# Performance work log

Hardware: AMD Instinct MI355X
Metric: run time of the kernel (lower is better)

Reference implementation:

```python
import jax, jax.numpy as jnp
import numpy as np

N = 8192
F_IN = 128
F_OUT = 128
NEG_SLOPE = 0.2


def setup_inputs() -> dict:
    key = jax.random.key(0)
    k_h, k_adj, k_W, k_a = jax.random.split(key, 4)
    h = jax.random.normal(k_h, (N, F_IN), dtype=jnp.float32)
    # binary adjacency mask as float (the module multiplies scores by adj)
    adj = (jax.random.uniform(k_adj, (N, N)) < 0.05).astype(jnp.float32)
    # nn.Linear(in, out, bias=False): weight shape [out, in]
    W = jax.random.normal(k_W, (F_OUT, F_IN), dtype=jnp.float32) / np.sqrt(F_IN)
    # nn.Linear(2*out, 1, bias=False): weight shape [1, 2*out]
    a = jax.random.normal(k_a, (1, 2 * F_OUT), dtype=jnp.float32) / np.sqrt(2 * F_OUT)
    return {"h": h, "adj": adj, "W": W, "a": a}


def reference(h, adj, W, a):
    # Wh: [N, F_out]
    Wh = h @ W.T
    f = Wh.shape[-1]
    # a([Wh_i ; Wh_j]) factored: e[i, j] = leaky_relu(Wh[i]@a1 + Wh[j]@a2)
    a1 = a[0, :f]  # [F_out]
    a2 = a[0, f:]  # [F_out]
    s_i = Wh @ a1  # [N]
    s_j = Wh @ a2  # [N]
    e = jax.nn.leaky_relu(s_i[:, None] + s_j[None, :], NEG_SLOPE)  # [N, N]
    # faithful to original: softmax over dim=1 of e * adj (multiplicative mask)
    attention = jax.nn.softmax(e * adj, axis=1)  # [N, N]
    return attention @ Wh  # [N, F_out]
```

## Files before the change

### kernel.cpp

```cpp
#include <hip/hip_runtime.h>

#define N_NODES 8192
#define FDIM 128
#define NEG_SLOPE 0.2f
#define SEG 512

__device__ __forceinline__ unsigned int f2bf(float f) {
  unsigned int u = __float_as_uint(f);
  return (u + 0x7FFFu + ((u >> 16) & 1u)) >> 16;
}

__global__ __launch_bounds__(256) void wh_fused_kernel(
    const float* __restrict__ h, const float* __restrict__ W,
    const float* __restrict__ a,
    unsigned int* __restrict__ Whb,
    float* __restrict__ s1, float* __restrict__ s2,
    float* __restrict__ S) {
  __shared__ float Wt[FDIM * 132];
  __shared__ float rows[32 * 132];
  const int t = threadIdx.x;
  const int base = blockIdx.x * 32;
  for (int it = 0; it < 64; ++it) {
    int idx = t + 256 * it;
    int o = idx >> 7, k = idx & 127;
    Wt[k * 132 + o] = W[idx];
  }
  for (int it = 0; it < 16; ++it) {
    int idx = t + 256 * it;
    int r = idx >> 7, col = idx & 127;
    rows[r * 132 + col] = h[(size_t)base * FDIM + idx];
  }
  __syncthreads();
  const int c4 = (t & 31) * 4;
  const int g = t >> 5;
  float acc[4][4];
#pragma unroll
  for (int rr = 0; rr < 4; ++rr)
#pragma unroll
    for (int cc = 0; cc < 4; ++cc) acc[rr][cc] = 0.f;
  for (int k = 0; k < FDIM; ++k) {
    float4 wv = *(const float4*)&Wt[k * 132 + c4];
    float rv[4];
#pragma unroll
    for (int rr = 0; rr < 4; ++rr) rv[rr] = rows[(4 * g + rr) * 132 + k];
#pragma unroll
    for (int rr = 0; rr < 4; ++rr) {
      acc[rr][0] += rv[rr] * wv.x;
      acc[rr][1] += rv[rr] * wv.y;
      acc[rr][2] += rv[rr] * wv.z;
      acc[rr][3] += rv[rr] * wv.w;
    }
  }
#pragma unroll
  for (int rr = 0; rr < 4; ++rr) {
    int r = base + 4 * g + rr;
    unsigned int p0 = f2bf(acc[rr][0]) | (f2bf(acc[rr][1]) << 16);
    unsigned int p1 = f2bf(acc[rr][2]) | (f2bf(acc[rr][3]) << 16);
    *(uint2*)&Whb[(size_t)r * 64 + (c4 >> 1)] = make_uint2(p0, p1);
  }
  {
    float4 a1v = *(const float4*)&a[c4];
    float4 a2v = *(const float4*)&a[FDIM + c4];
#pragma unroll
    for (int rr = 0; rr < 4; ++rr) {
      float d1 = acc[rr][0] * a1v.x + acc[rr][1] * a1v.y +
                 acc[rr][2] * a1v.z + acc[rr][3] * a1v.w;
      float d2 = acc[rr][0] * a2v.x + acc[rr][1] * a2v.y +
                 acc[rr][2] * a2v.z + acc[rr][3] * a2v.w;
#pragma unroll
      for (int off = 16; off; off >>= 1) {
        d1 += __shfl_down(d1, off);
        d2 += __shfl_down(d2, off);
      }
      if ((t & 31) == 0) {
        s1[base + 4 * g + rr] = d1;
        s2[base + 4 * g + rr] = d2;
      }
    }
  }
  __syncthreads();
  float4 cs = make_float4(acc[0][0] + acc[1][0] + acc[2][0] + acc[3][0],
                          acc[0][1] + acc[1][1] + acc[2][1] + acc[3][1],
                          acc[0][2] + acc[1][2] + acc[2][2] + acc[3][2],
                          acc[0][3] + acc[1][3] + acc[2][3] + acc[3][3]);
  *(float4*)&rows[g * FDIM + c4] = cs;
  __syncthreads();
  if (t < FDIM) {
    float s = 0.f;
#pragma unroll
    for (int gg = 0; gg < 8; ++gg) s += rows[gg * FDIM + t];
    atomicAdd(&S[t], s);
  }
}

__device__ __forceinline__ float4 ntload4(const float4* p) {
  typedef float f4v __attribute__((ext_vector_type(4)));
  f4v v = __builtin_nontemporal_load((const f4v*)p);
  return make_float4(v[0], v[1], v[2], v[3]);
}

__global__ __launch_bounds__(256, 4) void gat_row_kernel(
    const float* __restrict__ adj, const unsigned int* __restrict__ Whb,
    const float* __restrict__ s1, const float* __restrict__ s2,
    const float* __restrict__ S, float* __restrict__ out) {
  const int i = blockIdx.x;
  const int t = threadIdx.x;
  const int lane = t & 63;
  const int wave = t >> 6;
  __shared__ float2 pairs[4 * SEG];
  __shared__ int counts[4];
  __shared__ float red[4];
  __shared__ float red2[4];
  __shared__ float fpart[4][FDIM];

  const float s1i = s1[i];
  const float4* __restrict__ arow = (const float4*)(adj + (size_t)i * N_NODES);
  float2* __restrict__ mypairs = pairs + wave * SEG;
  const unsigned long long lmask = (1ull << lane) - 1ull;

  float4 av[8];
#pragma unroll
  for (int it = 0; it < 8; ++it) av[it] = ntload4(&arow[it * 256 + t]);
  asm volatile("" ::
      "v"(av[0].x), "v"(av[0].y), "v"(av[0].z), "v"(av[0].w),
      "v"(av[1].x), "v"(av[1].y), "v"(av[1].z), "v"(av[1].w),
      "v"(av[2].x), "v"(av[2].y), "v"(av[2].z), "v"(av[2].w),
      "v"(av[3].x), "v"(av[3].y), "v"(av[3].z), "v"(av[3].w),
      "v"(av[4].x), "v"(av[4].y), "v"(av[4].z), "v"(av[4].w),
      "v"(av[5].x), "v"(av[5].y), "v"(av[5].z), "v"(av[5].w),
      "v"(av[6].x), "v"(av[6].y), "v"(av[6].z), "v"(av[6].w),
      "v"(av[7].x), "v"(av[7].y), "v"(av[7].z), "v"(av[7].w));
  __builtin_amdgcn_sched_barrier(0);
  int cbase = 0;
#pragma unroll
  for (int it = 0; it < 8; ++it) {
    const int j4 = it * 256 + t;
    float v[4] = {av[it].x, av[it].y, av[it].z, av[it].w};
#pragma unroll
    for (int c = 0; c < 4; ++c) {
      bool pred = (v[c] != 0.f);
      unsigned long long b = __ballot(pred);
      if (pred) {
        int pos = cbase + (int)__popcll(b & lmask);
        if (pos < SEG) ((int*)&mypairs[pos])[1] = j4 * 4 + c;
      }
      cbase += (int)__popcll(b);
    }
  }
  const int mycnt = cbase < SEG ? cbase : SEG;
  if (lane == 0) counts[wave] = mycnt;

  float lmax = -1e30f;
  for (int k = lane; k < mycnt; k += 64) {
    int j = ((const int*)&mypairs[k])[1];
    float e = s1i + s2[j];
    e = e > 0.f ? e : NEG_SLOPE * e;
    mypairs[k].x = e;
    lmax = fmaxf(lmax, e);
  }
  for (int off = 32; off; off >>= 1) lmax = fmaxf(lmax, __shfl_down(lmax, off));
  if (lane == 0) red[wave] = lmax;
  __syncthreads();
  const int cnt = counts[0] + counts[1] + counts[2] + counts[3];
  float m = fmaxf(fmaxf(red[0], red[1]), fmaxf(red[2], red[3]));
  if (cnt < N_NODES) m = fmaxf(m, 0.f);
  const float em = __expf(-m);

  float lsum = 0.f;
  for (int k = lane; k < mycnt; k += 64) {
    float p = __expf(mypairs[k].x - m);
    mypairs[k].x = p;
    lsum += p;
  }
  for (int off = 32; off; off >>= 1) lsum += __shfl_down(lsum, off);
  if (lane == 0) red2[wave] = lsum;

  const int half = lane >> 5, lq = lane & 31;
  const uint2* __restrict__ Whb2 = (const uint2*)Whb;
  float ax = 0.f, ay = 0.f, az = 0.f, aw = 0.f;
  const int nit = (mycnt + 1) >> 1;
  int it = 0;
  for (; it + 3 < nit; it += 4) {
#pragma unroll
    for (int c = 0; c < 4; ++c) {
      int p = 2 * (it + c) + half;
      bool ok = p < mycnt;
      float2 pr = mypairs[ok ? p : 0];
      int j = ((const int*)&pr)[1];
      uint2 d = Whb2[((size_t)j << 5) + lq];
      float w = ok ? pr.x - em : 0.f;
      ax += w * __uint_as_float(d.x << 16);
      ay += w * __uint_as_float(d.x & 0xffff0000u);
      az += w * __uint_as_float(d.y << 16);
      aw += w * __uint_as_float(d.y & 0xffff0000u);
    }
  }
  for (; it < nit; ++it) {
    int p = 2 * it + half;
    bool ok = p < mycnt;
    float2 pr = mypairs[ok ? p : 0];
    int j = ((const int*)&pr)[1];
    uint2 d = Whb2[((size_t)j << 5) + lq];
    float w = ok ? pr.x - em : 0.f;
    ax += w * __uint_as_float(d.x << 16);
    ay += w * __uint_as_float(d.x & 0xffff0000u);
    az += w * __uint_as_float(d.y << 16);
    aw += w * __uint_as_float(d.y & 0xffff0000u);
  }
  ax += __shfl_down(ax, 32);
  ay += __shfl_down(ay, 32);
  az += __shfl_down(az, 32);
  aw += __shfl_down(aw, 32);
  if (lane < 32)
    *(float4*)&fpart[wave][4 * lq] = make_float4(ax, ay, az, aw);
  __syncthreads();
  if (t < FDIM) {
    float l = red2[0] + red2[1] + red2[2] + red2[3]
              + (float)(N_NODES - cnt) * em;
    float o = (fpart[0][t] + fpart[1][t] + fpart[2][t] + fpart[3][t]
               + em * S[t]) / l;
    out[(size_t)i * FDIM + t] = o;
  }
}

extern "C" void kernel_launch(void* const* d_in, const int* in_sizes, int n_in,
                              void* d_out, int out_size, void* d_ws, size_t ws_size,
                              hipStream_t stream) {
  const float* h   = (const float*)d_in[0];
  const float* adj = (const float*)d_in[1];
  const float* W   = (const float*)d_in[2];
  const float* a   = (const float*)d_in[3];
  float* out = (float*)d_out;
  unsigned int* Whb = (unsigned int*)d_ws;
  float* s1 = (float*)(Whb + (size_t)N_NODES * 64);
  float* s2 = s1 + N_NODES;
  float* S  = s2 + N_NODES;

  hipMemsetAsync(S, 0, FDIM * sizeof(float), stream);
  hipLaunchKernelGGL(wh_fused_kernel, dim3(N_NODES / 32), dim3(256), 0, stream,
                     h, W, a, Whb, s1, s2, S);
  hipLaunchKernelGGL(gat_row_kernel, dim3(N_NODES), dim3(256), 0, stream,
                     adj, Whb, s1, s2, S, out);
}
```

Before: 404.1 us.

## Fuse score computation into compaction and exp into aggregation; pre-transpose W

The row kernel now loads the whole s2 vector coalesced alongside the adjacency row and computes the leaky-relu scores and running max during the ballot compaction. This removes the separate gather pass over s2 and the separate exp/sum pass over the pair buffer, and the exp and sum now run inside the aggregation loop. The exp is evaluated once per half-wave lane, so lsum is scaled by 1/32. W is also transposed once in a small extra kernel so the projection kernel can use float4 loads. The cost is an extra 32 KB read of s2 per row and one more kernel launch.

```diff
diff --git a/kernel.cpp b/kernel.cpp
--- a/kernel.cpp
+++ b/kernel.cpp
@@ -10,8 +10,14 @@
   return (u + 0x7FFFu + ((u >> 16) & 1u)) >> 16;
 }
 
+__global__ __launch_bounds__(256) void transpose_w_kernel(
+    const float* __restrict__ W, float* __restrict__ WtG) {
+  int idx = blockIdx.x * 256 + threadIdx.x;
+  WtG[idx] = W[(idx & 127) * FDIM + (idx >> 7)];
+}
+
 __global__ __launch_bounds__(256) void wh_fused_kernel(
-    const float* __restrict__ h, const float* __restrict__ W,
+    const float* __restrict__ h, const float* __restrict__ WtG,
     const float* __restrict__ a,
     unsigned int* __restrict__ Whb,
     float* __restrict__ s1, float* __restrict__ s2,
@@ -20,15 +26,16 @@
   __shared__ float rows[32 * 132];
   const int t = threadIdx.x;
   const int base = blockIdx.x * 32;
-  for (int it = 0; it < 64; ++it) {
-    int idx = t + 256 * it;
-    int o = idx >> 7, k = idx & 127;
-    Wt[k * 132 + o] = W[idx];
-  }
   for (int it = 0; it < 16; ++it) {
     int idx = t + 256 * it;
-    int r = idx >> 7, col = idx & 127;
-    rows[r * 132 + col] = h[(size_t)base * FDIM + idx];
+    int k = idx >> 5, c = (idx & 31) * 4;
+    *(float4*)&Wt[k * 132 + c] = *(const float4*)&WtG[k * FDIM + c];
+  }
+  for (int it = 0; it < 4; ++it) {
+    int idx = t + 256 * it;
+    int r = idx >> 5, c = (idx & 31) * 4;
+    *(float4*)&rows[r * 132 + c] =
+        *(const float4*)&h[(size_t)(base + r) * FDIM + c];
   }
   __syncthreads();
   const int c4 = (t & 31) * 4;
@@ -97,6 +104,11 @@
   typedef float f4v __attribute__((ext_vector_type(4)));
   f4v v = __builtin_nontemporal_load((const f4v*)p);
   return make_float4(v[0], v[1], v[2], v[3]);
+}
+
+__device__ __forceinline__ int mbcnt64(unsigned long long b) {
+  return (int)__builtin_amdgcn_mbcnt_hi(
+      (unsigned)(b >> 32), __builtin_amdgcn_mbcnt_lo((unsigned)b, 0u));
 }
 
 __global__ __launch_bounds__(256, 4) void gat_row_kernel(
@@ -115,49 +127,42 @@
 
   const float s1i = s1[i];
   const float4* __restrict__ arow = (const float4*)(adj + (size_t)i * N_NODES);
+  const float4* __restrict__ srow = (const float4*)s2;
   float2* __restrict__ mypairs = pairs + wave * SEG;
-  const unsigned long long lmask = (1ull << lane) - 1ull;
-
-  float4 av[8];
+
+  float4 av[8], sv[8];
 #pragma unroll
   for (int it = 0; it < 8; ++it) av[it] = ntload4(&arow[it * 256 + t]);
-  asm volatile("" ::
-      "v"(av[0].x), "v"(av[0].y), "v"(av[0].z), "v"(av[0].w),
-      "v"(av[1].x), "v"(av[1].y), "v"(av[1].z), "v"(av[1].w),
-      "v"(av[2].x), "v"(av[2].y), "v"(av[2].z), "v"(av[2].w),
-      "v"(av[3].x), "v"(av[3].y), "v"(av[3].z), "v"(av[3].w),
-      "v"(av[4].x), "v"(av[4].y), "v"(av[4].z), "v"(av[4].w),
-      "v"(av[5].x), "v"(av[5].y), "v"(av[5].z), "v"(av[5].w),
-      "v"(av[6].x), "v"(av[6].y), "v"(av[6].z), "v"(av[6].w),
-      "v"(av[7].x), "v"(av[7].y), "v"(av[7].z), "v"(av[7].w));
-  __builtin_amdgcn_sched_barrier(0);
+#pragma unroll
+  for (int it = 0; it < 8; ++it) sv[it] = srow[it * 256 + t];
   int cbase = 0;
+  float lmax = -1e30f;
 #pragma unroll
   for (int it = 0; it < 8; ++it) {
     const int j4 = it * 256 + t;
-    float v[4] = {av[it].x, av[it].y, av[it].z, av[it].w};
+    float vv[4] = {av[it].x, av[it].y, av[it].z, av[it].w};
+    float ss[4] = {sv[it].x, sv[it].y, sv[it].z, sv[it].w};
 #pragma unroll
     for (int c = 0; c < 4; ++c) {
-      bool pred = (v[c] != 0.f);
+      bool pred = (vv[c] != 0.f);
+      float e = s1i + ss[c];
+      e = e > 0.f ? e : NEG_SLOPE * e;
       unsigned long long b = __ballot(pred);
       if (pred) {
-        int pos = cbase + (int)__popcll(b & lmask);
-        if (pos < SEG) ((int*)&mypairs[pos])[1] = j4 * 4 + c;
+        int pos = cbase + mbcnt64(b);
+        if (pos < SEG) {
+          float2 pr;
+          pr.x = e;
+          ((int*)&pr)[1] = j4 * 4 + c;
+          mypairs[pos] = pr;
+        }
       }
+      lmax = fmaxf(lmax, pred ? e : -1e30f);
       cbase += (int)__popcll(b);
     }
   }
   const int mycnt = cbase < SEG ? cbase : SEG;
   if (lane == 0) counts[wave] = mycnt;
-
-  float lmax = -1e30f;
-  for (int k = lane; k < mycnt; k += 64) {
-    int j = ((const int*)&mypairs[k])[1];
-    float e = s1i + s2[j];
-    e = e > 0.f ? e : NEG_SLOPE * e;
-    mypairs[k].x = e;
-    lmax = fmaxf(lmax, e);
-  }
   for (int off = 32; off; off >>= 1) lmax = fmaxf(lmax, __shfl_down(lmax, off));
   if (lane == 0) red[wave] = lmax;
   __syncthreads();
@@ -166,18 +171,9 @@
   if (cnt < N_NODES) m = fmaxf(m, 0.f);
   const float em = __expf(-m);
 
-  float lsum = 0.f;
-  for (int k = lane; k < mycnt; k += 64) {
-    float p = __expf(mypairs[k].x - m);
-    mypairs[k].x = p;
-    lsum += p;
-  }
-  for (int off = 32; off; off >>= 1) lsum += __shfl_down(lsum, off);
-  if (lane == 0) red2[wave] = lsum;
-
   const int half = lane >> 5, lq = lane & 31;
   const uint2* __restrict__ Whb2 = (const uint2*)Whb;
-  float ax = 0.f, ay = 0.f, az = 0.f, aw = 0.f;
+  float ax = 0.f, ay = 0.f, az = 0.f, aw = 0.f, lsum = 0.f;
   const int nit = (mycnt + 1) >> 1;
   int it = 0;
   for (; it + 3 < nit; it += 4) {
@@ -188,7 +184,9 @@
       float2 pr = mypairs[ok ? p : 0];
       int j = ((const int*)&pr)[1];
       uint2 d = Whb2[((size_t)j << 5) + lq];
-      float w = ok ? pr.x - em : 0.f;
+      float pv = __expf(pr.x - m);
+      float w = ok ? pv - em : 0.f;
+      lsum += ok ? pv : 0.f;
       ax += w * __uint_as_float(d.x << 16);
       ay += w * __uint_as_float(d.x & 0xffff0000u);
       az += w * __uint_as_float(d.y << 16);
@@ -201,12 +199,16 @@
     float2 pr = mypairs[ok ? p : 0];
     int j = ((const int*)&pr)[1];
     uint2 d = Whb2[((size_t)j << 5) + lq];
-    float w = ok ? pr.x - em : 0.f;
+    float pv = __expf(pr.x - m);
+    float w = ok ? pv - em : 0.f;
+    lsum += ok ? pv : 0.f;
     ax += w * __uint_as_float(d.x << 16);
     ay += w * __uint_as_float(d.x & 0xffff0000u);
     az += w * __uint_as_float(d.y << 16);
     aw += w * __uint_as_float(d.y & 0xffff0000u);
   }
+  for (int off = 32; off; off >>= 1) lsum += __shfl_down(lsum, off);
+  if (lane == 0) red2[wave] = lsum * (1.f / 32.f);
   ax += __shfl_down(ax, 32);
   ay += __shfl_down(ay, 32);
   az += __shfl_down(az, 32);
@@ -232,13 +234,16 @@
   const float* a   = (const float*)d_in[3];
   float* out = (float*)d_out;
   unsigned int* Whb = (unsigned int*)d_ws;
-  float* s1 = (float*)(Whb + (size_t)N_NODES * 64);
-  float* s2 = s1 + N_NODES;
-  float* S  = s2 + N_NODES;
+  float* s1  = (float*)(Whb + (size_t)N_NODES * 64);
+  float* s2  = s1 + N_NODES;
+  float* S   = s2 + N_NODES;
+  float* WtG = S + FDIM;
 
   hipMemsetAsync(S, 0, FDIM * sizeof(float), stream);
+  hipLaunchKernelGGL(transpose_w_kernel, dim3(FDIM * FDIM / 256), dim3(256), 0,
+                     stream, W, WtG);
   hipLaunchKernelGGL(wh_fused_kernel, dim3(N_NODES / 32), dim3(256), 0, stream,
-                     h, W, a, Whb, s1, s2, S);
+                     h, WtG, a, Whb, s1, s2, S);
   hipLaunchKernelGGL(gat_row_kernel, dim3(N_NODES), dim3(256), 0, stream,
                      adj, Whb, s1, s2, S, out);
 }
```

Result: no change. 410.2 us (+1.5%).
